# Kernel optimization log

Hardware: AMD Instinct MI355X
Metric: run time of the kernel (lower is better)

Reference implementation:

```python
import jax, jax.numpy as jnp
import numpy as np

N = 50000      # nodes
E = 600000     # edges
F_IN = 11      # QM9 node features
H = 128        # hidden_channels
L = 5          # num_layers
G = 2048       # number of graphs in batch
EPS = 1e-5


def setup_inputs() -> dict:
    key = jax.random.key(0)
    ks = jax.random.split(key, 12)
    x = jax.random.normal(ks[0], (N, F_IN), dtype=jnp.float32)
    edge_index = jax.random.randint(ks[1], (2, E), 0, N, dtype=jnp.int64)
    batch = jnp.sort(jax.random.randint(ks[2], (N,), 0, G, dtype=jnp.int64))
    W0 = jax.random.normal(ks[3], (F_IN, H), dtype=jnp.float32) * 0.1
    b0 = jnp.zeros((H,), jnp.float32)
    Ws = jax.random.normal(ks[4], (L - 1, H, H), dtype=jnp.float32) * 0.05
    bs = jnp.zeros((L - 1, H), jnp.float32)
    bn_gamma = jnp.ones((L, H), jnp.float32)
    bn_beta = jnp.zeros((L, H), jnp.float32)
    bn_mean = jax.random.normal(ks[5], (L, H), dtype=jnp.float32) * 0.1
    bn_var = jax.random.uniform(ks[6], (L, H), minval=0.5, maxval=1.5, dtype=jnp.float32)
    lin1_w = jax.random.normal(ks[7], (H, H // 2), dtype=jnp.float32) * 0.05
    lin1_b = jnp.zeros((H // 2,), jnp.float32)
    lin2_w = jax.random.normal(ks[8], (H // 2, 1), dtype=jnp.float32) * 0.1
    lin2_b = jnp.zeros((1,), jnp.float32)
    return {"x": x, "edge_index": edge_index, "batch": batch,
            "W0": W0, "b0": b0, "Ws": Ws, "bs": bs,
            "bn_gamma": bn_gamma, "bn_beta": bn_beta,
            "bn_mean": bn_mean, "bn_var": bn_var,
            "lin1_w": lin1_w, "lin1_b": lin1_b,
            "lin2_w": lin2_w, "lin2_b": lin2_b}


def reference(x, edge_index, batch, W0, b0, Ws, bs, bn_gamma, bn_beta,
              bn_mean, bn_var, lin1_w, lin1_b, lin2_w, lin2_b):
    n = x.shape[0]
    # --- add self-loops (PyG GCNConv default) ---
    loop = jnp.arange(n, dtype=edge_index.dtype)
    src = jnp.concatenate([edge_index[0], loop])
    dst = jnp.concatenate([edge_index[1], loop])
    # symmetric normalization: deg over dst including self-loops (>=1)
    deg = jax.ops.segment_sum(jnp.ones(src.shape[0], x.dtype), dst, num_segments=n)
    dinv = jax.lax.rsqrt(deg)
    norm = (dinv[src] * dinv[dst])[:, None]  # [E+N, 1]

    for i in range(L):
        W = W0 if i == 0 else Ws[i - 1]
        b = b0 if i == 0 else bs[i - 1]
        h = x @ W                                            # [N, H]
        agg = jax.ops.segment_sum(h[src] * norm, dst, num_segments=n) + b
        # BatchNorm (eval mode: running stats) + ReLU
        xb = (agg - bn_mean[i]) * jax.lax.rsqrt(bn_var[i] + EPS) * bn_gamma[i] + bn_beta[i]
        xn = jax.nn.relu(xb)
        # residual only when shapes match and i > 0
        x = x + xn if (i > 0 and x.shape[-1] == xn.shape[-1]) else xn

    # --- global mean pool over graph ids ---
    sums = jax.ops.segment_sum(x, batch, num_segments=G)          # [G, H]
    cnts = jax.ops.segment_sum(jnp.ones((n,), x.dtype), batch, num_segments=G)
    pooled = sums / jnp.maximum(cnts, 1.0)[:, None]
    # dropout is identity in inference
    h1 = jax.nn.relu(pooled @ lin1_w + lin1_b)
    out = h1 @ lin2_w + lin2_b                                    # [G, 1]
    return out
```

## Files before the change

kernel.cpp:

```cpp
#include <hip/hip_runtime.h>

#define HDIM 128
#define BN_EPS 1e-5f


__global__ void k_zero2(int* __restrict__ a, int* __restrict__ b, int n) {
    int i = blockIdx.x * blockDim.x + threadIdx.x;
    if (i < n) { a[i] = 0; b[i] = 0; }
}

__global__ void k_deg_accum(const int* __restrict__ dst, int* __restrict__ deg, int e) {
    int i = blockIdx.x * blockDim.x + threadIdx.x;
    if (i < e) atomicAdd(&deg[dst[i]], 1);
}

__global__ void k_dinv(const int* __restrict__ deg, float* __restrict__ dinv, int n) {
    int i = blockIdx.x * blockDim.x + threadIdx.x;
    if (i < n) dinv[i] = rsqrtf((float)deg[i] + 1.0f);
}

__global__ void k_scan1(const int* __restrict__ deg, int* __restrict__ rs,
                        int* __restrict__ blk, int n) {
    __shared__ int s[256];
    int i = blockIdx.x * 256 + threadIdx.x;
    int v = (i < n) ? deg[i] : 0;
    s[threadIdx.x] = v;
    __syncthreads();
    for (int off = 1; off < 256; off <<= 1) {
        int t = (threadIdx.x >= off) ? s[threadIdx.x - off] : 0;
        __syncthreads();
        s[threadIdx.x] += t;
        __syncthreads();
    }
    if (i < n) rs[i] = s[threadIdx.x] - v;
    if (threadIdx.x == 255) blk[blockIdx.x] = s[255];
}

__global__ void k_scan2(int* __restrict__ blk, int nb) {
    __shared__ int s[256];
    int t = threadIdx.x;
    int v = (t < nb) ? blk[t] : 0;
    s[t] = v;
    __syncthreads();
    for (int off = 1; off < 256; off <<= 1) {
        int u = (t >= off) ? s[t - off] : 0;
        __syncthreads();
        s[t] += u;
        __syncthreads();
    }
    if (t < nb) blk[t] = s[t] - v;
}

__global__ void k_scan3(int* __restrict__ rs, const int* __restrict__ blk, int n) {
    int i = blockIdx.x * 256 + threadIdx.x;
    if (i < n) rs[i] += blk[blockIdx.x];
}

__global__ void k_fill(const int* __restrict__ src, const int* __restrict__ dst,
                       const int* __restrict__ rs, int* __restrict__ cur,
                       int* __restrict__ csr, int e) {
    int i = blockIdx.x * blockDim.x + threadIdx.x;
    if (i >= e) return;
    int d = dst[i];
    int pos = rs[d] + atomicAdd(&cur[d], 1);
    csr[pos] = src[i];
}

__global__ void k_bounds(const int* __restrict__ batch, int* __restrict__ bnd,
                         int n, int g) {
    int i = blockIdx.x * blockDim.x + threadIdx.x;
    if (i >= n) return;
    int b = batch[i];
    if (i == 0) {
        for (int q = 0; q <= b; ++q) bnd[q] = 0;
    } else {
        int p = batch[i - 1];
        for (int q = p + 1; q <= b; ++q) bnd[q] = i;
    }
    if (i == n - 1) {
        for (int q = b + 1; q <= g; ++q) bnd[q] = n;
    }
}

__global__ __launch_bounds__(256) void k_gemm0(
    const float* __restrict__ x, const float* __restrict__ W,
    const float* __restrict__ dinv, float* __restrict__ hs, int n, int fin) {
    int row = blockIdx.x * 2 + (threadIdx.x >> 7);
    int f = threadIdx.x & 127;
    if (row >= n) return;
    float acc = 0.0f;
    for (int k = 0; k < fin; ++k)
        acc += x[row * fin + k] * W[k * HDIM + f];
    hs[row * HDIM + f] = acc * dinv[row];
}

__global__ __launch_bounds__(256) void k_gemm(
    const float* __restrict__ x, const float* __restrict__ W,
    const float* __restrict__ dinv, float* __restrict__ hs, int n) {
    __shared__ float xs[64][HDIM];
    int row0 = blockIdx.x * 64;
    int tid = threadIdx.x;

    #pragma unroll
    for (int j = 0; j < 8; ++j) {
        int fid = tid + 256 * j;
        int r = fid >> 5, k4 = fid & 31;
        float4 v = make_float4(0.f, 0.f, 0.f, 0.f);
        int gr = row0 + r;
        if (gr < n) v = *(const float4*)(x + (size_t)gr * HDIM + k4 * 4);
        *(float4*)(&xs[r][k4 * 4]) = v;
    }
    __syncthreads();

    int rg = tid >> 5;
    int cg = tid & 31;
    float4 acc[8];
    #pragma unroll
    for (int r = 0; r < 8; ++r) acc[r] = make_float4(0.f, 0.f, 0.f, 0.f);

    for (int kk = 0; kk < HDIM; kk += 4) {
        float4 wv[4];
        #pragma unroll
        for (int k = 0; k < 4; ++k)
            wv[k] = *(const float4*)(W + (size_t)(kk + k) * HDIM + cg * 4);
        #pragma unroll
        for (int r = 0; r < 8; ++r) {
            float4 xv = *(const float4*)(&xs[rg * 8 + r][kk]);
            acc[r].x += xv.x * wv[0].x + xv.y * wv[1].x + xv.z * wv[2].x + xv.w * wv[3].x;
            acc[r].y += xv.x * wv[0].y + xv.y * wv[1].y + xv.z * wv[2].y + xv.w * wv[3].y;
            acc[r].z += xv.x * wv[0].z + xv.y * wv[1].z + xv.z * wv[2].z + xv.w * wv[3].z;
            acc[r].w += xv.x * wv[0].w + xv.y * wv[1].w + xv.z * wv[2].w + xv.w * wv[3].w;
        }
    }

    #pragma unroll
    for (int r = 0; r < 8; ++r) {
        int gr = row0 + rg * 8 + r;
        if (gr < n) {
            float s = dinv[gr];
            float4 o = make_float4(acc[r].x * s, acc[r].y * s, acc[r].z * s, acc[r].w * s);
            *(float4*)(hs + (size_t)gr * HDIM + cg * 4) = o;
        }
    }
}

__global__ __launch_bounds__(256) void k_agg(
    const int* __restrict__ rs, const int* __restrict__ deg,
    const int* __restrict__ csr, const float* __restrict__ hs,
    const float* __restrict__ dinv, const float* __restrict__ bias,
    const float* __restrict__ gamma, const float* __restrict__ beta,
    const float* __restrict__ mean, const float* __restrict__ var,
    const float* __restrict__ xold, float* __restrict__ xnew,
    int n, int use_res) {
    int node = blockIdx.x * 8 + (threadIdx.x >> 5);
    if (node >= n) return;
    int f4 = (threadIdx.x & 31) * 4;
    size_t base = (size_t)node * HDIM + f4;

    float4 a0 = *(const float4*)(hs + base);
    float4 a1 = make_float4(0.f, 0.f, 0.f, 0.f);
    float4 a2 = make_float4(0.f, 0.f, 0.f, 0.f);
    float4 a3 = make_float4(0.f, 0.f, 0.f, 0.f);
    int start = rs[node];
    int d = deg[node];
    int j = 0;
    for (; j + 4 <= d; j += 4) {
        int s0 = csr[start + j];
        int s1 = csr[start + j + 1];
        int s2 = csr[start + j + 2];
        int s3 = csr[start + j + 3];
        float4 v0 = *(const float4*)(hs + (size_t)s0 * HDIM + f4);
        float4 v1 = *(const float4*)(hs + (size_t)s1 * HDIM + f4);
        float4 v2 = *(const float4*)(hs + (size_t)s2 * HDIM + f4);
        float4 v3 = *(const float4*)(hs + (size_t)s3 * HDIM + f4);
        a0.x += v0.x; a0.y += v0.y; a0.z += v0.z; a0.w += v0.w;
        a1.x += v1.x; a1.y += v1.y; a1.z += v1.z; a1.w += v1.w;
        a2.x += v2.x; a2.y += v2.y; a2.z += v2.z; a2.w += v2.w;
        a3.x += v3.x; a3.y += v3.y; a3.z += v3.z; a3.w += v3.w;
    }
    for (; j < d; ++j) {
        int s0 = csr[start + j];
        float4 v0 = *(const float4*)(hs + (size_t)s0 * HDIM + f4);
        a0.x += v0.x; a0.y += v0.y; a0.z += v0.z; a0.w += v0.w;
    }
    float4 acc;
    acc.x = (a0.x + a1.x) + (a2.x + a3.x);
    acc.y = (a0.y + a1.y) + (a2.y + a3.y);
    acc.z = (a0.z + a1.z) + (a2.z + a3.z);
    acc.w = (a0.w + a1.w) + (a2.w + a3.w);

    float di = dinv[node];
    float4 bv = *(const float4*)(bias + f4);
    float4 gv = *(const float4*)(gamma + f4);
    float4 be = *(const float4*)(beta + f4);
    float4 mv = *(const float4*)(mean + f4);
    float4 vv = *(const float4*)(var + f4);
    float4 o;
    o.x = fmaxf((di * acc.x + bv.x - mv.x) * rsqrtf(vv.x + BN_EPS) * gv.x + be.x, 0.f);
    o.y = fmaxf((di * acc.y + bv.y - mv.y) * rsqrtf(vv.y + BN_EPS) * gv.y + be.y, 0.f);
    o.z = fmaxf((di * acc.z + bv.z - mv.z) * rsqrtf(vv.z + BN_EPS) * gv.z + be.z, 0.f);
    o.w = fmaxf((di * acc.w + bv.w - mv.w) * rsqrtf(vv.w + BN_EPS) * gv.w + be.w, 0.f);
    if (use_res) {
        float4 xo = *(const float4*)(xold + base);
        o.x += xo.x; o.y += xo.y; o.z += xo.z; o.w += xo.w;
    }
    *(float4*)(xnew + base) = o;
}

__global__ __launch_bounds__(256) void k_pool_seg(
    const float* __restrict__ x, const int* __restrict__ bnd,
    float* __restrict__ pooled, int g) {
    int gid = blockIdx.x * 8 + (threadIdx.x >> 5);
    if (gid >= g) return;
    int f4 = (threadIdx.x & 31) * 4;
    int s = bnd[gid], t = bnd[gid + 1];
    float4 a0 = make_float4(0.f, 0.f, 0.f, 0.f);
    float4 a1 = make_float4(0.f, 0.f, 0.f, 0.f);
    int r = s;
    for (; r + 2 <= t; r += 2) {
        float4 v0 = *(const float4*)(x + (size_t)r * HDIM + f4);
        float4 v1 = *(const float4*)(x + (size_t)(r + 1) * HDIM + f4);
        a0.x += v0.x; a0.y += v0.y; a0.z += v0.z; a0.w += v0.w;
        a1.x += v1.x; a1.y += v1.y; a1.z += v1.z; a1.w += v1.w;
    }
    if (r < t) {
        float4 v0 = *(const float4*)(x + (size_t)r * HDIM + f4);
        a0.x += v0.x; a0.y += v0.y; a0.z += v0.z; a0.w += v0.w;
    }
    float inv = (t > s) ? 1.0f / (float)(t - s) : 0.0f;
    float4 o = make_float4((a0.x + a1.x) * inv, (a0.y + a1.y) * inv,
                           (a0.z + a1.z) * inv, (a0.w + a1.w) * inv);
    *(float4*)(pooled + (size_t)gid * HDIM + f4) = o;
}

__global__ __launch_bounds__(64) void k_head(
    const float* __restrict__ pooled,
    const float* __restrict__ w1, const float* __restrict__ b1,
    const float* __restrict__ w2, const float* __restrict__ b2,
    float* __restrict__ out) {
    __shared__ float p[HDIM];
    int g = blockIdx.x;
    int t = threadIdx.x;
    p[t]      = pooled[(size_t)g * HDIM + t];
    p[t + 64] = pooled[(size_t)g * HDIM + 64 + t];
    __syncthreads();
    float h = b1[t];
    #pragma unroll 4
    for (int k = 0; k < HDIM; ++k)
        h += p[k] * w1[k * 64 + t];
    h = fmaxf(h, 0.f);
    float part = h * w2[t];
    #pragma unroll
    for (int off = 32; off > 0; off >>= 1)
        part += __shfl_down(part, off);
    if (t == 0) out[g] = part + b2[0];
}

extern "C" void kernel_launch(void* const* d_in, const int* in_sizes, int n_in,
                              void* d_out, int out_size, void* d_ws, size_t ws_size,
                              hipStream_t stream) {
    const float* x0   = (const float*)d_in[0];
    const int*   eidx = (const int*)  d_in[1];
    const int*   batch= (const int*)  d_in[2];
    const float* W0   = (const float*)d_in[3];
    const float* b0   = (const float*)d_in[4];
    const float* Ws   = (const float*)d_in[5];
    const float* bs   = (const float*)d_in[6];
    const float* gam  = (const float*)d_in[7];
    const float* bet  = (const float*)d_in[8];
    const float* mean = (const float*)d_in[9];
    const float* var  = (const float*)d_in[10];
    const float* w1   = (const float*)d_in[11];
    const float* b1   = (const float*)d_in[12];
    const float* w2   = (const float*)d_in[13];
    const float* b2   = (const float*)d_in[14];

    const int FIN = 11;
    int n = in_sizes[0] / FIN;
    int e = in_sizes[1] / 2;
    int g = out_size;
    int nb = (n + 255) / 256;

    const int* src = eidx;
    const int* dst = eidx + e;

    char* ws = (char*)d_ws;
    size_t nal = ((size_t)n + 255) & ~(size_t)255;
    int*   deg   = (int*)ws;                       ws += nal * 4;
    int*   cur   = (int*)ws;                       ws += nal * 4;
    int*   rs    = (int*)ws;                       ws += nal * 4;
    int*   blk   = (int*)ws;                       ws += 256 * 4;
    int*   bnd   = (int*)ws;                       ws += ((size_t)g + 64) / 64 * 64 * 4;
    int*   csr   = (int*)ws;                       ws += ((size_t)e + 63) / 64 * 64 * 4;
    float* dinv  = (float*)ws;                     ws += nal * 4;
    float* bufA  = (float*)ws;                     ws += (size_t)n * HDIM * 4;
    float* bufB  = (float*)ws;                     ws += (size_t)n * HDIM * 4;
    float* pooled= (float*)ws;

    k_zero2<<<nb, 256, 0, stream>>>(deg, cur, n);
    k_deg_accum<<<(e + 255) / 256, 256, 0, stream>>>(dst, deg, e);
    k_dinv<<<nb, 256, 0, stream>>>(deg, dinv, n);
    k_scan1<<<nb, 256, 0, stream>>>(deg, rs, blk, n);
    k_scan2<<<1, 256, 0, stream>>>(blk, nb);
    k_scan3<<<nb, 256, 0, stream>>>(rs, blk, n);
    k_fill<<<(e + 255) / 256, 256, 0, stream>>>(src, dst, rs, cur, csr, e);
    k_bounds<<<nb, 256, 0, stream>>>(batch, bnd, n, g);

    for (int i = 0; i < 5; ++i) {
        const float* xin = (i == 0) ? x0 : bufA;
        const float* bias = (i == 0) ? b0 : bs + (size_t)(i - 1) * HDIM;
        if (i == 0) {
            k_gemm0<<<(n + 1) / 2, 256, 0, stream>>>(x0, W0, dinv, bufB, n, FIN);
        } else {
            const float* W = Ws + (size_t)(i - 1) * HDIM * HDIM;
            k_gemm<<<(n + 63) / 64, 256, 0, stream>>>(bufA, W, dinv, bufB, n);
        }
        k_agg<<<(n + 7) / 8, 256, 0, stream>>>(
            rs, deg, csr, bufB, dinv, bias,
            gam + i * HDIM, bet + i * HDIM, mean + i * HDIM, var + i * HDIM,
            xin, bufA, n, (i > 0) ? 1 : 0);
    }

    k_pool_seg<<<(g + 7) / 8, 256, 0, stream>>>(bufA, bnd, pooled, g);
    k_head<<<g, 64, 0, stream>>>(pooled, w1, b1, w2, b2, (float*)d_out);
}
```

Before: 588.5 us.

## Use fp16 features with MFMA GEMM and feature-sliced aggregation

Stores the transformed node features in fp16 and replaces the fp32 SIMT GEMM with an MFMA 16x16x32 f16 kernel that reads a transposed fp16 copy of each weight matrix. The aggregation kernel also writes an fp16 copy of its output for the next layer's GEMM. Its grid is reorganized so each block covers 64 nodes times one 16-feature slice, which is meant to improve cache locality of the gathers. This halves the gather traffic and uses matrix cores, at the cost of fp16 rounding in the features and an extra weight conversion kernel per layer.

```diff
diff --git a/kernel.cpp b/kernel.cpp
--- a/kernel.cpp
+++ b/kernel.cpp
@@ -1,7 +1,22 @@
 #include <hip/hip_runtime.h>
+#include <hip/hip_fp16.h>
 
 #define HDIM 128
 #define BN_EPS 1e-5f
+
+typedef _Float16 f16x8 __attribute__((ext_vector_type(8)));
+typedef _Float16 f16x4 __attribute__((ext_vector_type(4)));
+typedef float    f32x4 __attribute__((ext_vector_type(4)));
+
+__device__ inline float4 ld_h4(const _Float16* p) {
+    f16x4 r = *(const f16x4*)p;
+    return make_float4((float)r.x, (float)r.y, (float)r.z, (float)r.w);
+}
+
+__device__ inline void st_h4(_Float16* p, float4 v) {
+    f16x4 o = { (_Float16)v.x, (_Float16)v.y, (_Float16)v.z, (_Float16)v.w };
+    *(f16x4*)p = o;
+}
 
 
 __global__ void k_zero2(int* __restrict__ a, int* __restrict__ b, int n) {
@@ -82,82 +97,74 @@
     }
 }
 
+__global__ __launch_bounds__(256) void k_wconv(const float* __restrict__ W,
+                                               _Float16* __restrict__ wt) {
+    int idx = blockIdx.x * 256 + threadIdx.x;
+    int k = idx >> 7, c = idx & 127;
+    wt[(size_t)c * HDIM + k] = (_Float16)W[(size_t)k * HDIM + c];
+}
+
 __global__ __launch_bounds__(256) void k_gemm0(
     const float* __restrict__ x, const float* __restrict__ W,
-    const float* __restrict__ dinv, float* __restrict__ hs, int n, int fin) {
+    const float* __restrict__ dinv, _Float16* __restrict__ hs, int n, int fin) {
     int row = blockIdx.x * 2 + (threadIdx.x >> 7);
     int f = threadIdx.x & 127;
     if (row >= n) return;
     float acc = 0.0f;
     for (int k = 0; k < fin; ++k)
         acc += x[row * fin + k] * W[k * HDIM + f];
-    hs[row * HDIM + f] = acc * dinv[row];
-}
-
-__global__ __launch_bounds__(256) void k_gemm(
-    const float* __restrict__ x, const float* __restrict__ W,
-    const float* __restrict__ dinv, float* __restrict__ hs, int n) {
-    __shared__ float xs[64][HDIM];
-    int row0 = blockIdx.x * 64;
-    int tid = threadIdx.x;
-
+    hs[(size_t)row * HDIM + f] = (_Float16)(acc * dinv[row]);
+}
+
+__global__ __launch_bounds__(256) void k_gemm_mfma(
+    const _Float16* __restrict__ xh, const _Float16* __restrict__ wt,
+    const float* __restrict__ dinv, _Float16* __restrict__ hs, int n) {
+    int wid  = threadIdx.x >> 6;
+    int lane = threadIdx.x & 63;
+    int xr   = blockIdx.x * 64 + wid * 16 + (lane & 15);
+    int kc   = (lane >> 4) * 8;
+
+    f32x4 acc[8];
     #pragma unroll
-    for (int j = 0; j < 8; ++j) {
-        int fid = tid + 256 * j;
-        int r = fid >> 5, k4 = fid & 31;
-        float4 v = make_float4(0.f, 0.f, 0.f, 0.f);
-        int gr = row0 + r;
-        if (gr < n) v = *(const float4*)(x + (size_t)gr * HDIM + k4 * 4);
-        *(float4*)(&xs[r][k4 * 4]) = v;
-    }
-    __syncthreads();
-
-    int rg = tid >> 5;
-    int cg = tid & 31;
-    float4 acc[8];
+    for (int t = 0; t < 8; ++t) acc[t] = (f32x4){0.f, 0.f, 0.f, 0.f};
+
     #pragma unroll
-    for (int r = 0; r < 8; ++r) acc[r] = make_float4(0.f, 0.f, 0.f, 0.f);
-
-    for (int kk = 0; kk < HDIM; kk += 4) {
-        float4 wv[4];
+    for (int kb = 0; kb < HDIM; kb += 32) {
+        f16x8 bfrag = {};
+        if (xr < n) bfrag = *(const f16x8*)(xh + (size_t)xr * HDIM + kb + kc);
         #pragma unroll
-        for (int k = 0; k < 4; ++k)
-            wv[k] = *(const float4*)(W + (size_t)(kk + k) * HDIM + cg * 4);
-        #pragma unroll
-        for (int r = 0; r < 8; ++r) {
-            float4 xv = *(const float4*)(&xs[rg * 8 + r][kk]);
-            acc[r].x += xv.x * wv[0].x + xv.y * wv[1].x + xv.z * wv[2].x + xv.w * wv[3].x;
-            acc[r].y += xv.x * wv[0].y + xv.y * wv[1].y + xv.z * wv[2].y + xv.w * wv[3].y;
-            acc[r].z += xv.x * wv[0].z + xv.y * wv[1].z + xv.z * wv[2].z + xv.w * wv[3].z;
-            acc[r].w += xv.x * wv[0].w + xv.y * wv[1].w + xv.z * wv[2].w + xv.w * wv[3].w;
+        for (int t = 0; t < 8; ++t) {
+            f16x8 afrag = *(const f16x8*)(wt + (size_t)(t * 16 + (lane & 15)) * HDIM + kb + kc);
+            acc[t] = __builtin_amdgcn_mfma_f32_16x16x32_f16(afrag, bfrag, acc[t], 0, 0, 0);
         }
     }
 
+    if (xr >= n) return;
+    float di = dinv[xr];
     #pragma unroll
-    for (int r = 0; r < 8; ++r) {
-        int gr = row0 + rg * 8 + r;
-        if (gr < n) {
-            float s = dinv[gr];
-            float4 o = make_float4(acc[r].x * s, acc[r].y * s, acc[r].z * s, acc[r].w * s);
-            *(float4*)(hs + (size_t)gr * HDIM + cg * 4) = o;
-        }
+    for (int t = 0; t < 8; ++t) {
+        int c0 = t * 16 + (lane >> 4) * 4;
+        f16x4 o = { (_Float16)(acc[t][0] * di), (_Float16)(acc[t][1] * di),
+                    (_Float16)(acc[t][2] * di), (_Float16)(acc[t][3] * di) };
+        *(f16x4*)(hs + (size_t)xr * HDIM + c0) = o;
     }
 }
 
 __global__ __launch_bounds__(256) void k_agg(
     const int* __restrict__ rs, const int* __restrict__ deg,
-    const int* __restrict__ csr, const float* __restrict__ hs,
+    const int* __restrict__ csr, const _Float16* __restrict__ hs,
     const float* __restrict__ dinv, const float* __restrict__ bias,
     const float* __restrict__ gamma, const float* __restrict__ beta,
     const float* __restrict__ mean, const float* __restrict__ var,
     const float* __restrict__ xold, float* __restrict__ xnew,
-    int n, int use_res) {
-    int node = blockIdx.x * 8 + (threadIdx.x >> 5);
+    _Float16* __restrict__ xh, int n, int use_res) {
+    int slice = blockIdx.x & 7;
+    int node  = (blockIdx.x >> 3) * 64 + (threadIdx.x >> 2);
     if (node >= n) return;
-    int f4 = (threadIdx.x & 31) * 4;
-    size_t base = (size_t)node * HDIM + f4;
-
-    float4 a0 = *(const float4*)(hs + base);
+    int f = slice * 16 + (threadIdx.x & 3) * 4;
+    size_t base = (size_t)node * HDIM + f;
+
+    float4 a0 = ld_h4(hs + base);
     float4 a1 = make_float4(0.f, 0.f, 0.f, 0.f);
     float4 a2 = make_float4(0.f, 0.f, 0.f, 0.f);
     float4 a3 = make_float4(0.f, 0.f, 0.f, 0.f);
@@ -169,10 +176,10 @@
         int s1 = csr[start + j + 1];
         int s2 = csr[start + j + 2];
         int s3 = csr[start + j + 3];
-        float4 v0 = *(const float4*)(hs + (size_t)s0 * HDIM + f4);
-        float4 v1 = *(const float4*)(hs + (size_t)s1 * HDIM + f4);
-        float4 v2 = *(const float4*)(hs + (size_t)s2 * HDIM + f4);
-        float4 v3 = *(const float4*)(hs + (size_t)s3 * HDIM + f4);
+        float4 v0 = ld_h4(hs + (size_t)s0 * HDIM + f);
+        float4 v1 = ld_h4(hs + (size_t)s1 * HDIM + f);
+        float4 v2 = ld_h4(hs + (size_t)s2 * HDIM + f);
+        float4 v3 = ld_h4(hs + (size_t)s3 * HDIM + f);
         a0.x += v0.x; a0.y += v0.y; a0.z += v0.z; a0.w += v0.w;
         a1.x += v1.x; a1.y += v1.y; a1.z += v1.z; a1.w += v1.w;
         a2.x += v2.x; a2.y += v2.y; a2.z += v2.z; a2.w += v2.w;
@@ -180,7 +187,7 @@
     }
     for (; j < d; ++j) {
         int s0 = csr[start + j];
-        float4 v0 = *(const float4*)(hs + (size_t)s0 * HDIM + f4);
+        float4 v0 = ld_h4(hs + (size_t)s0 * HDIM + f);
         a0.x += v0.x; a0.y += v0.y; a0.z += v0.z; a0.w += v0.w;
     }
     float4 acc;
@@ -190,11 +197,11 @@
     acc.w = (a0.w + a1.w) + (a2.w + a3.w);
 
     float di = dinv[node];
-    float4 bv = *(const float4*)(bias + f4);
-    float4 gv = *(const float4*)(gamma + f4);
-    float4 be = *(const float4*)(beta + f4);
-    float4 mv = *(const float4*)(mean + f4);
-    float4 vv = *(const float4*)(var + f4);
+    float4 bv = *(const float4*)(bias + f);
+    float4 gv = *(const float4*)(gamma + f);
+    float4 be = *(const float4*)(beta + f);
+    float4 mv = *(const float4*)(mean + f);
+    float4 vv = *(const float4*)(var + f);
     float4 o;
     o.x = fmaxf((di * acc.x + bv.x - mv.x) * rsqrtf(vv.x + BN_EPS) * gv.x + be.x, 0.f);
     o.y = fmaxf((di * acc.y + bv.y - mv.y) * rsqrtf(vv.y + BN_EPS) * gv.y + be.y, 0.f);
@@ -205,6 +212,7 @@
         o.x += xo.x; o.y += xo.y; o.z += xo.z; o.w += xo.w;
     }
     *(float4*)(xnew + base) = o;
+    st_h4(xh + base, o);
 }
 
 __global__ __launch_bounds__(256) void k_pool_seg(
@@ -286,16 +294,18 @@
 
     char* ws = (char*)d_ws;
     size_t nal = ((size_t)n + 255) & ~(size_t)255;
-    int*   deg   = (int*)ws;                       ws += nal * 4;
-    int*   cur   = (int*)ws;                       ws += nal * 4;
-    int*   rs    = (int*)ws;                       ws += nal * 4;
-    int*   blk   = (int*)ws;                       ws += 256 * 4;
-    int*   bnd   = (int*)ws;                       ws += ((size_t)g + 64) / 64 * 64 * 4;
-    int*   csr   = (int*)ws;                       ws += ((size_t)e + 63) / 64 * 64 * 4;
-    float* dinv  = (float*)ws;                     ws += nal * 4;
-    float* bufA  = (float*)ws;                     ws += (size_t)n * HDIM * 4;
-    float* bufB  = (float*)ws;                     ws += (size_t)n * HDIM * 4;
-    float* pooled= (float*)ws;
+    int*      deg   = (int*)ws;                    ws += nal * 4;
+    int*      cur   = (int*)ws;                    ws += nal * 4;
+    int*      rs    = (int*)ws;                    ws += nal * 4;
+    int*      blk   = (int*)ws;                    ws += 256 * 4;
+    int*      bnd   = (int*)ws;                    ws += ((size_t)g + 64) / 64 * 64 * 4;
+    int*      csr   = (int*)ws;                    ws += ((size_t)e + 63) / 64 * 64 * 4;
+    float*    dinv  = (float*)ws;                  ws += nal * 4;
+    _Float16* wt    = (_Float16*)ws;               ws += (size_t)HDIM * HDIM * 2;
+    float*    bufA  = (float*)ws;                  ws += (size_t)n * HDIM * 4;
+    _Float16* bufH  = (_Float16*)ws;               ws += (size_t)n * HDIM * 2;
+    _Float16* xh    = (_Float16*)ws;               ws += (size_t)n * HDIM * 2;
+    float*    pooled= (float*)ws;
 
     k_zero2<<<nb, 256, 0, stream>>>(deg, cur, n);
     k_deg_accum<<<(e + 255) / 256, 256, 0, stream>>>(dst, deg, e);
@@ -306,19 +316,22 @@
     k_fill<<<(e + 255) / 256, 256, 0, stream>>>(src, dst, rs, cur, csr, e);
     k_bounds<<<nb, 256, 0, stream>>>(batch, bnd, n, g);
 
+    int aggGrid = ((n + 63) / 64) * 8;
+
     for (int i = 0; i < 5; ++i) {
         const float* xin = (i == 0) ? x0 : bufA;
         const float* bias = (i == 0) ? b0 : bs + (size_t)(i - 1) * HDIM;
         if (i == 0) {
-            k_gemm0<<<(n + 1) / 2, 256, 0, stream>>>(x0, W0, dinv, bufB, n, FIN);
+            k_gemm0<<<(n + 1) / 2, 256, 0, stream>>>(x0, W0, dinv, bufH, n, FIN);
         } else {
             const float* W = Ws + (size_t)(i - 1) * HDIM * HDIM;
-            k_gemm<<<(n + 63) / 64, 256, 0, stream>>>(bufA, W, dinv, bufB, n);
+            k_wconv<<<64, 256, 0, stream>>>(W, wt);
+            k_gemm_mfma<<<(n + 63) / 64, 256, 0, stream>>>(xh, wt, dinv, bufH, n);
         }
-        k_agg<<<(n + 7) / 8, 256, 0, stream>>>(
-            rs, deg, csr, bufB, dinv, bias,
+        k_agg<<<aggGrid, 256, 0, stream>>>(
+            rs, deg, csr, bufH, dinv, bias,
             gam + i * HDIM, bet + i * HDIM, mean + i * HDIM, var + i * HDIM,
-            xin, bufA, n, (i > 0) ? 1 : 0);
+            xin, bufA, xh, n, (i > 0) ? 1 : 0);
     }
 
     k_pool_seg<<<(g + 7) / 8, 256, 0, stream>>>(bufA, bnd, pooled, g);
```

Measured after the change: 661.2 us. 12.4% more time.
